# Optimization experiments

Hardware: AMD Instinct MI355X
Metric: run time of the kernel (lower is better)

The kernel has to match this reference:

```python
import jax, jax.numpy as jnp
import numpy as np

B = 4          # clouds per batch
N_PER = 8192   # points per cloud
RATIO = 0.5
M = int(N_PER * RATIO)   # sampled centroids per cloud
R = 0.2        # radius
K = 64         # max_num_neighbors
C_IN = 64


def setup_inputs() -> dict:
    key = jax.random.key(0)
    k1, k2, k3, k4 = jax.random.split(key, 4)
    N = B * N_PER
    x = jax.random.normal(k1, (N, C_IN), dtype=jnp.float32)
    pos = jax.random.uniform(k2, (N, 3), dtype=jnp.float32)  # unit cube
    batch = jnp.repeat(jnp.arange(B, dtype=jnp.int32), N_PER)
    W1 = jax.random.normal(k3, (C_IN + 3, 64), dtype=jnp.float32) * (1.0 / np.sqrt(C_IN + 3))
    b1 = jnp.zeros((64,), dtype=jnp.float32)
    W2 = jax.random.normal(k4, (64, 128), dtype=jnp.float32) * (1.0 / np.sqrt(64))
    b2 = jnp.zeros((128,), dtype=jnp.float32)
    return {"x": x, "pos": pos, "batch": batch, "W1": W1, "b1": b1, "W2": W2, "b2": b2}


def _fps(posb):
    """Farthest point sampling, vectorized over clouds. posb: [B, n, 3] -> idx [B, M]."""
    d0 = jnp.sum((posb - posb[:, :1]) ** 2, axis=-1)  # dist^2 to seed point 0: [B, n]

    def step(dists, _):
        far = jnp.argmax(dists, axis=1)                              # [B]
        newp = jnp.take_along_axis(posb, far[:, None, None], axis=1)  # [B, 1, 3]
        d = jnp.sum((posb - newp) ** 2, axis=-1)                      # [B, n]
        return jnp.minimum(dists, d), far.astype(jnp.int32)

    _, rest = jax.lax.scan(step, d0, None, length=M - 1)  # rest: [M-1, B]
    return jnp.concatenate([jnp.zeros((B, 1), jnp.int32), rest.T], axis=1)  # [B, M]


def reference(x, pos, batch, W1, b1, W2, b2):
    posb = pos.reshape(B, N_PER, 3)
    xb = x.reshape(B, N_PER, C_IN)

    # --- fps ---
    idx = _fps(posb)                                         # [B, M]
    q = jnp.take_along_axis(posb, idx[:, :, None], axis=1)   # sampled centroids [B, M, 3]

    # --- radius query: K nearest neighbors within radius R (same cloud) ---
    d2 = jnp.sum((q[:, :, None, :] - posb[:, None, :, :]) ** 2, axis=-1)  # [B, M, n]
    neg = jnp.where(d2 <= R * R, -d2, -jnp.inf)
    vals, nbr = jax.lax.top_k(neg, K)                        # [B, M, K]
    valid = vals > -jnp.inf                                  # neighbor mask

    # --- PointNetConv: gather -> MLP -> masked max aggregation ---
    bidx = jnp.arange(B)[:, None, None]
    xj = xb[bidx, nbr]                                       # [B, M, K, C_IN]
    rel = posb[bidx, nbr] - q[:, :, None, :]                 # [B, M, K, 3]
    feat = jnp.concatenate([xj, rel], axis=-1)               # [B, M, K, C_IN+3]
    h = jax.nn.relu(feat @ W1 + b1)                          # [B, M, K, 64]
    h = jax.nn.relu(h @ W2 + b2)                             # [B, M, K, 128]
    h = jnp.where(valid[..., None], h, -jnp.inf)
    out = jnp.max(h, axis=2)                                 # [B, M, 128]; self-edge guarantees >=1 valid

    x_out = out.reshape(B * M, 128)
    pos_out = q.reshape(B * M, 3)
    batch_out = jnp.repeat(jnp.arange(B, dtype=batch.dtype), M)
    return x_out, pos_out, batch_out
```

## Files before the change

### kernel.cpp

```cpp
#include <hip/hip_runtime.h>
#include <stdint.h>

#define NPER 8192
#define NB 4
#define MPER 4096
#define MTOT (NB*MPER)
#define KNB 64
#define CIN 64
#define R2C 0.04f

#define POSOUT_OFF (MTOT*128)
#define BATCH_OFF  (MTOT*128 + MTOT*3)

#define SSTR 30720

typedef float v2f __attribute__((ext_vector_type(2)));

#define FPS_T 1024
#define PTS 8
#define NCELL 512

#define OFF_XS 0
#define OFF_YS (OFF_XS + NPER*4)
#define OFF_ZS (OFF_YS + NPER*4)
#define OFF_OS (OFF_ZS + NPER*4)
#define OFF_WIN (OFF_OS + NPER*2)
#define OFF_HIST (OFF_WIN + MPER*2)
#define OFF_SCAN (OFF_HIST + NCELL*4)
#define OFF_SLOT (OFF_SCAN + NCELL*4)
#define OFF_SID0 (OFF_SLOT + 24)
#define FPS_LDS  (OFF_SID0 + 8)

template<int CTRL>
__device__ __forceinline__ unsigned dppmax(unsigned v) {
  unsigned t = (unsigned)__builtin_amdgcn_update_dpp(
      0, (int)v, CTRL, 0xf, 0xf, true);
  return v > t ? v : t;
}
__device__ __forceinline__ unsigned wave_max_u32(unsigned v) {
  v = dppmax<0x111>(v);
  v = dppmax<0x112>(v);
  v = dppmax<0x114>(v);
  v = dppmax<0x118>(v);
  v = dppmax<0x142>(v);
  v = dppmax<0x143>(v);
  return (unsigned)__builtin_amdgcn_readlane((int)v, 63);
}

__global__ __launch_bounds__(1024) void k_fps(const float* __restrict__ pos,
                                              float* __restrict__ dout)
{
#pragma clang fp contract(off)
  extern __shared__ char smem[];
  float* Xs = (float*)(smem + OFF_XS);
  float* Ys = (float*)(smem + OFF_YS);
  float* Zs = (float*)(smem + OFF_ZS);
  unsigned short* Os = (unsigned short*)(smem + OFF_OS);
  unsigned short* winb = (unsigned short*)(smem + OFF_WIN);
  unsigned* hist = (unsigned*)(smem + OFF_HIST);
  unsigned* scanb = (unsigned*)(smem + OFF_SCAN);
  unsigned long long* slot3 = (unsigned long long*)(smem + OFF_SLOT);
  unsigned* sid0p = (unsigned*)(smem + OFF_SID0);

  const int b = blockIdx.x;
  const int tid = threadIdx.x;
  const float* pb = pos + (size_t)b * NPER * 3;
  float* qo = dout + POSOUT_OFF + (size_t)b * MPER * 3;
  float* scrb = dout + (size_t)b * SSTR;
  float* gSX = scrb; float* gSY = scrb + 8192; float* gSZ = scrb + 16384;
  unsigned* gSO = (unsigned*)(scrb + 24576);
  unsigned* gCS = (unsigned*)(scrb + 28672);

  if (tid < NCELL) hist[tid] = 0u;
  if (tid == 0) { slot3[0] = 0ull; slot3[1] = 0ull; slot3[2] = 0ull; }
  __syncthreads();

  float sxv[PTS], syv[PTS], szv[PTS];
  unsigned cellv[PTS];
#pragma unroll
  for (int k = 0; k < PTS; ++k) {
    int i = k * FPS_T + tid;
    sxv[k] = pb[i*3+0]; syv[k] = pb[i*3+1]; szv[k] = pb[i*3+2];
    unsigned ix = min(7u, (unsigned)(int)(sxv[k] * 8.0f));
    unsigned iy = min(7u, (unsigned)(int)(syv[k] * 8.0f));
    unsigned iz = min(7u, (unsigned)(int)(szv[k] * 8.0f));
    cellv[k] = (ix << 6) | (iy << 3) | iz;
    atomicAdd(&hist[cellv[k]], 1u);
  }
  __syncthreads();
  if (tid < NCELL) scanb[tid] = hist[tid];
  __syncthreads();
  for (int s = 1; s < NCELL; s <<= 1) {
    unsigned v = 0u;
    if (tid >= s && tid < NCELL) v = scanb[tid - s];
    __syncthreads();
    if (tid >= s && tid < NCELL) scanb[tid] += v;
    __syncthreads();
  }
  if (tid < NCELL) {
    hist[tid] = scanb[tid] - hist[tid];
    gCS[tid+1] = scanb[tid];
  }
  if (tid == 0) gCS[0] = 0u;
  __syncthreads();
#pragma unroll
  for (int k = 0; k < PTS; ++k) {
    unsigned dst = atomicAdd(&hist[cellv[k]], 1u);
    int orig = k * FPS_T + tid;
    Xs[dst] = sxv[k]; Ys[dst] = syv[k]; Zs[dst] = szv[k];
    Os[dst] = (unsigned short)orig;
    if (orig == 0) *sid0p = dst;
  }
  __syncthreads();
  for (int e = tid; e < NPER; e += FPS_T) {
    gSX[e] = Xs[e]; gSY[e] = Ys[e]; gSZ[e] = Zs[e];
  }
  for (int e = tid; e < NPER/2; e += FPS_T)
    gSO[e] = ((const unsigned*)Os)[e];
  v2f Xp[4], Yp[4], Zp[4], Dp[4];
  unsigned RK[PTS];
  float bxlo = 3.402823466e+38f, bylo = bxlo, bzlo = bxlo;
  float bxhi = -bxlo, byhi = bxhi, bzhi = bxhi;
#pragma unroll
  for (int k = 0; k < PTS; ++k) {
    int s = tid * PTS + k;
    float xx = Xs[s], yy = Ys[s], zz = Zs[s];
    Xp[k>>1][k&1] = xx; Yp[k>>1][k&1] = yy; Zp[k>>1][k&1] = zz;
    Dp[k>>1][k&1] = 3.402823466e+38f;
    unsigned orig = Os[s];
    RK[k] = ((unsigned)(NPER - 1 - orig) << 13) | (unsigned)s;
    bxlo = fminf(bxlo, xx); bxhi = fmaxf(bxhi, xx);
    bylo = fminf(bylo, yy); byhi = fmaxf(byhi, yy);
    bzlo = fminf(bzlo, zz); bzhi = fmaxf(bzhi, zz);
  }

  unsigned long long tkey = 0ull, wkey = 0ull;
  float lmax = 3.402823466e+38f;
  unsigned sidx = *sid0p;
  for (int m = 1; m < MPER; ++m) {
    const float cx = Xs[sidx], cy = Ys[sidx], cz = Zs[sidx];
    if (tid == 0) winb[m-1] = (unsigned short)sidx;
    if (tid == 1) slot3[(m+1) % 3] = 0ull;
    float ax = fmaxf(fmaxf(__fsub_rn(bxlo, cx), __fsub_rn(cx, bxhi)), 0.0f);
    float ay = fmaxf(fmaxf(__fsub_rn(bylo, cy), __fsub_rn(cy, byhi)), 0.0f);
    float az = fmaxf(fmaxf(__fsub_rn(bzlo, cz), __fsub_rn(cz, bzhi)), 0.0f);
    float lb = ax*ax + ay*ay + az*az;
    bool upd = (lb * 0.99988f) < lmax;
    if (__ballot(upd) != 0ull) {
      if (upd) {
        v2f cx2 = {cx, cx}, cy2 = {cy, cy}, cz2 = {cz, cz};
        v2f dnp[4];
        float bd = -1.0f;
#pragma unroll
        for (int p = 0; p < 4; ++p) {
          v2f dx = Xp[p] - cx2;
          v2f dy = Yp[p] - cy2;
          v2f dz = Zp[p] - cz2;
          v2f s = (dx*dx + dy*dy) + dz*dz;
          v2f dn;
          dn.x = fminf(Dp[p].x, s.x);
          dn.y = fminf(Dp[p].y, s.y);
          Dp[p] = dn; dnp[p] = dn;
          bd = fmaxf(bd, fmaxf(dn.x, dn.y));
        }
        unsigned brk = 0u;
#pragma unroll
        for (int p = 0; p < 4; ++p) {
          brk = (dnp[p].x == bd) ? max(brk, RK[2*p])   : brk;
          brk = (dnp[p].y == bd) ? max(brk, RK[2*p+1]) : brk;
        }
        tkey = ((unsigned long long)__float_as_uint(bd) << 26) | brk;
        lmax = bd;
      }
      unsigned hi = (unsigned)(tkey >> 26);
      unsigned M = wave_max_u32(hi);
      unsigned rk = (unsigned)tkey & 0x3FFFFFFu;
      unsigned long long msk = __ballot(hi == M);
      unsigned lo;
      if (__popcll(msk) == 1) {
        int ln = (int)__builtin_ctzll(msk);
        lo = (unsigned)__builtin_amdgcn_readlane((int)rk, ln);
      } else {
        lo = wave_max_u32((hi == M) ? rk : 0u);
      }
      wkey = ((unsigned long long)M << 26) | lo;
    }
    if ((tid & 63) == 0) atomicMax(&slot3[m % 3], wkey);
    __syncthreads();
    sidx = (unsigned)(slot3[m % 3] & 0x1FFFull);
  }
  if (tid == 0) winb[MPER-1] = (unsigned short)sidx;
  __syncthreads();
  for (int e = tid; e < MPER; e += FPS_T) {
    unsigned s = winb[e];
    qo[e*3+0] = Xs[s]; qo[e*3+1] = Ys[s]; qo[e*3+2] = Zs[s];
  }
}

#define SCAP 512
__global__ __launch_bounds__(256) void k_radius(const float* __restrict__ pos,
    float* __restrict__ dout, unsigned short* __restrict__ nbr,
    int* __restrict__ cnt)
{
  __shared__ unsigned candH[4][SCAP];
  __shared__ unsigned candL[4][SCAP];
  const int wid = threadIdx.x >> 6, lane = threadIdx.x & 63;
  const int m = blockIdx.x * 4 + wid;
  const int b = m >> 12;
  const float* scrb = dout + (size_t)b * SSTR;
  const float* SX = scrb;
  const float* SY = scrb + 8192;
  const float* SZ = scrb + 16384;
  const unsigned short* SO = (const unsigned short*)(scrb + 24576);
  const unsigned* CS = (const unsigned*)(scrb + 28672);
  const float* q = dout + POSOUT_OFF + (size_t)m * 3;
  const float qx = q[0], qy = q[1], qz = q[2];
  const int ixc = min(7, (int)(qx * 8.0f));
  const int iyc = min(7, (int)(qy * 8.0f));
  const int izc = min(7, (int)(qz * 8.0f));
  const int izlo = max(izc-2, 0), izhi = min(izc+2, 7);
  unsigned s0v = 0u, s1v = 0u;
  {
    int ix = ixc + lane / 5 - 2;
    int iy = iyc + lane % 5 - 2;
    if (lane < 25 && ix >= 0 && ix < 8 && iy >= 0 && iy < 8) {
      int cb = (ix << 6) | (iy << 3);
      s0v = CS[cb + izlo];
      s1v = CS[cb + izhi + 1];
    }
  }
  unsigned cw = 0;
  for (int seg = 0; seg < 25; ++seg) {
    unsigned s0 = (unsigned)__builtin_amdgcn_readlane((int)s0v, seg);
    unsigned s1 = (unsigned)__builtin_amdgcn_readlane((int)s1v, seg);
    for (unsigned i0 = s0; i0 < s1; i0 += 64) {
      unsigned i = i0 + (unsigned)lane;
      float dx = __fsub_rn(qx, SX[i]);
      float dy = __fsub_rn(qy, SY[i]);
      float dz = __fsub_rn(qz, SZ[i]);
      float d2 = __fadd_rn(__fadd_rn(__fmul_rn(dx,dx), __fmul_rn(dy,dy)),
                           __fmul_rn(dz,dz));
      bool in = (i < s1) && (d2 <= R2C);
      unsigned long long mk = __ballot(in);
      unsigned pre = (unsigned)__popcll(mk & ((1ull << lane) - 1ull));
      if (in) {
        unsigned slot = cw + pre;
        if (slot < SCAP) {
          candH[wid][slot] = __float_as_uint(d2);
          candL[wid][slot] = (unsigned)SO[i];
        }
      }
      cw += (unsigned)__popcll(mk);
    }
  }
  if (cw > SCAP) cw = SCAP;
  for (int s = (int)cw + lane; s < SCAP; s += 64) {
    candH[wid][s] = 0xFFFFFFFFu; candL[wid][s] = 0xFFFFFFFFu;
  }
  __syncthreads();
  for (int k = 2; k <= SCAP; k <<= 1) {
    for (int j = k >> 1; j > 0; j >>= 1) {
#pragma unroll
      for (int s = 0; s < SCAP/128; ++s) {
        int t = lane + (s << 6);
        int e = ((t & ~(j-1)) << 1) | (t & (j-1));
        int p = e | j;
        unsigned aH = candH[wid][e], aL = candL[wid][e];
        unsigned cH = candH[wid][p], cL = candL[wid][p];
        bool agt = (aH > cH) || (aH == cH && aL > cL);
        bool asc = ((e & k) == 0);
        bool sw = asc ? agt : !agt && (aH != cH || aL != cL);
        if (sw) {
          candH[wid][e] = cH; candL[wid][e] = cL;
          candH[wid][p] = aH; candL[wid][p] = aL;
        }
      }
      __syncthreads();
    }
  }
  int kk = (int)cw; if (kk > KNB) kk = KNB;
  nbr[(size_t)m*KNB + lane] =
    (lane < kk) ? (unsigned short)(candL[wid][lane] & 0xFFFFu)
                : (unsigned short)0;
  if (lane == 0) {
    cnt[m] = kk;
    dout[BATCH_OFF + m] = (float)b;
  }
}

__global__ __launch_bounds__(128) void k_conv(
    const float* __restrict__ x, const float* __restrict__ pos,
    const float* __restrict__ W1, const float* __restrict__ b1,
    const float* __restrict__ W2, const float* __restrict__ b2,
    const unsigned short* __restrict__ nbr, const int* __restrict__ cntp,
    float* __restrict__ dout)
{
  __shared__ __align__(16) float bufA[68*68];
  __shared__ __align__(16) float bufB[68*68];
  __shared__ unsigned short nbr_s[64];
  __shared__ float qv[3];
  __shared__ int cnt_s;
  const int t = threadIdx.x;
  const int m = blockIdx.x;
  const int b = m >> 12;
  if (t < 64) nbr_s[t] = nbr[(size_t)m*KNB + t];
  else if (t == 64) cnt_s = cntp[m];
  else if (t >= 65 && t < 68) qv[t-65] = dout[POSOUT_OFF + (size_t)m*3 + (t-65)];
  for (int e = t; e < 67*64; e += 128) {
    int ch = e >> 6, h = e & 63;
    bufB[ch*68 + h] = W1[e];
  }
  __syncthreads();
  {
    const int ch = t & 63, jj = t >> 6;
    const size_t xb = (size_t)b * NPER * CIN;
    for (int j0 = 0; j0 < 64; j0 += 2) {
      int j = j0 + jj;
      int r = nbr_s[j];
      bufA[ch*68 + j] = x[xb + (size_t)r*CIN + ch];
    }
  }
  {
    const size_t pbb = (size_t)b * NPER * 3;
    for (int e = t; e < 192; e += 128) {
      int j = e & 63, d = e >> 6;
      int r = nbr_s[j];
      bufA[(64+d)*68 + j] = pos[pbb + (size_t)r*3 + d] - qv[d];
    }
  }
  __syncthreads();

  const int jg = t & 7, hg = t >> 3;
  const int j0 = jg << 3;
  const int h0 = hg << 2;
  float acc[4][8];
#pragma unroll
  for (int hh = 0; hh < 4; ++hh)
#pragma unroll
    for (int j = 0; j < 8; ++j) acc[hh][j] = 0.0f;
  for (int ch = 0; ch < 67; ++ch) {
    const float4 fa = *(const float4*)&bufA[ch*68 + j0];
    const float4 fb = *(const float4*)&bufA[ch*68 + j0 + 4];
    const float4 w  = *(const float4*)&bufB[ch*68 + h0];
    const float ws4[4] = {w.x, w.y, w.z, w.w};
    const float fj[8] = {fa.x, fa.y, fa.z, fa.w, fb.x, fb.y, fb.z, fb.w};
#pragma unroll
    for (int hh = 0; hh < 4; ++hh)
#pragma unroll
      for (int j = 0; j < 8; ++j)
        acc[hh][j] += ws4[hh] * fj[j];
  }
  __syncthreads();
  {
    const float4 bb = *(const float4*)&b1[h0];
    const float bv[4] = {bb.x, bb.y, bb.z, bb.w};
#pragma unroll
    for (int hh = 0; hh < 4; ++hh) {
      float4 o0, o1;
      o0.x = fmaxf(acc[hh][0] + bv[hh], 0.0f);
      o0.y = fmaxf(acc[hh][1] + bv[hh], 0.0f);
      o0.z = fmaxf(acc[hh][2] + bv[hh], 0.0f);
      o0.w = fmaxf(acc[hh][3] + bv[hh], 0.0f);
      o1.x = fmaxf(acc[hh][4] + bv[hh], 0.0f);
      o1.y = fmaxf(acc[hh][5] + bv[hh], 0.0f);
      o1.z = fmaxf(acc[hh][6] + bv[hh], 0.0f);
      o1.w = fmaxf(acc[hh][7] + bv[hh], 0.0f);
      *(float4*)&bufA[(h0+hh)*68 + j0] = o0;
      *(float4*)&bufA[(h0+hh)*68 + j0 + 4] = o1;
    }
  }
  const int c0 = hg << 3;
  float acc2[8][8];
#pragma unroll
  for (int c = 0; c < 8; ++c)
#pragma unroll
    for (int j = 0; j < 8; ++j) acc2[c][j] = 0.0f;
  for (int hc = 0; hc < 64; hc += 16) {
    __syncthreads();
    for (int e = t; e < 16*128; e += 128) {
      int hh = e >> 7, c = e & 127;
      bufB[hh*136 + c] = W2[(size_t)(hc+hh)*128 + c];
    }
    __syncthreads();
#pragma unroll
    for (int h = 0; h < 16; ++h) {
      const float4 ja = *(const float4*)&bufA[(hc+h)*68 + j0];
      const float4 jb = *(const float4*)&bufA[(hc+h)*68 + j0 + 4];
      const float4 wa = *(const float4*)&bufB[h*136 + c0];
      const float4 wb = *(const float4*)&bufB[h*136 + c0 + 4];
      const float hv[8] = {ja.x, ja.y, ja.z, ja.w, jb.x, jb.y, jb.z, jb.w};
      const float wv[8] = {wa.x, wa.y, wa.z, wa.w, wb.x, wb.y, wb.z, wb.w};
#pragma unroll
      for (int c = 0; c < 8; ++c)
#pragma unroll
        for (int j = 0; j < 8; ++j)
          acc2[c][j] += wv[c] * hv[j];
    }
  }
  const int cntv = cnt_s;
  const float4 b2a = *(const float4*)&b2[c0];
  const float4 b2b = *(const float4*)&b2[c0 + 4];
  const float bv2[8] = {b2a.x, b2a.y, b2a.z, b2a.w, b2b.x, b2b.y, b2b.z, b2b.w};
  float best[8];
#pragma unroll
  for (int c = 0; c < 8; ++c) {
    float v = -3.402823466e+38f;
#pragma unroll
    for (int j = 0; j < 8; ++j) {
      float hv = fmaxf(acc2[c][j] + bv2[c], 0.0f);
      v = (j0 + j < cntv) ? fmaxf(v, hv) : v;
    }
    best[c] = v;
  }
#pragma unroll
  for (int off = 1; off < 8; off <<= 1)
#pragma unroll
    for (int c = 0; c < 8; ++c)
      best[c] = fmaxf(best[c], __shfl_xor(best[c], off));
  if (jg == 0) {
    float4 o0 = {best[0], best[1], best[2], best[3]};
    float4 o1 = {best[4], best[5], best[6], best[7]};
    *(float4*)&dout[(size_t)m*128 + c0] = o0;
    *(float4*)&dout[(size_t)m*128 + c0 + 4] = o1;
  }
}

extern "C" void kernel_launch(void* const* d_in, const int* in_sizes, int n_in,
                              void* d_out, int out_size, void* d_ws, size_t ws_size,
                              hipStream_t stream) {
  const float* x   = (const float*)d_in[0];
  const float* pos = (const float*)d_in[1];
  const float* W1  = (const float*)d_in[3];
  const float* b1  = (const float*)d_in[4];
  const float* W2  = (const float*)d_in[5];
  const float* b2  = (const float*)d_in[6];
  float* dout = (float*)d_out;
  unsigned short* nbr = (unsigned short*)d_ws;
  int* cnt = (int*)((char*)d_ws + (size_t)MTOT*KNB*2);

  hipLaunchKernelGGL(k_fps,    dim3(NB),     dim3(FPS_T), FPS_LDS, stream, pos, dout);
  hipLaunchKernelGGL(k_radius, dim3(MTOT/4), dim3(256),   0, stream, pos, dout, nbr, cnt);
  hipLaunchKernelGGL(k_conv,   dim3(MTOT),   dim3(128),   0, stream,
                     x, pos, W1, b1, W2, b2, nbr, cnt, dout);
}
```

Baseline: 3.354 ms.

## Use bounding-sphere skip test in FPS, interleave xyz, pack MLP FMAs

The FPS loop replaces the per-thread AABB lower-bound test with a bounding-sphere test. It precomputes a threshold from the thread's max min-distance, so the skip check costs one squared distance against the sphere centre. Point coordinates in LDS move from three SoA arrays to an interleaved xyz array, so each centroid fetch reads adjacent words. The MLP kernel's two GEMM inner loops are rewritten with v2f accumulators to encourage packed FP32 FMA instructions. The sphere bound is looser than the box bound, so more threads may do the update step.

New measurement: 4.646 ms. 1.39x slower.

```diff
diff --git a/kernel.cpp b/kernel.cpp
--- a/kernel.cpp
+++ b/kernel.cpp
@@ -20,10 +20,8 @@
 #define PTS 8
 #define NCELL 512
 
-#define OFF_XS 0
-#define OFF_YS (OFF_XS + NPER*4)
-#define OFF_ZS (OFF_YS + NPER*4)
-#define OFF_OS (OFF_ZS + NPER*4)
+#define OFF_XYZ 0
+#define OFF_OS (OFF_XYZ + NPER*12)
 #define OFF_WIN (OFF_OS + NPER*2)
 #define OFF_HIST (OFF_WIN + MPER*2)
 #define OFF_SCAN (OFF_HIST + NCELL*4)
@@ -52,9 +50,7 @@
 {
 #pragma clang fp contract(off)
   extern __shared__ char smem[];
-  float* Xs = (float*)(smem + OFF_XS);
-  float* Ys = (float*)(smem + OFF_YS);
-  float* Zs = (float*)(smem + OFF_ZS);
+  float* xyz = (float*)(smem + OFF_XYZ);
   unsigned short* Os = (unsigned short*)(smem + OFF_OS);
   unsigned short* winb = (unsigned short*)(smem + OFF_WIN);
   unsigned* hist = (unsigned*)(smem + OFF_HIST);
@@ -107,13 +103,13 @@
   for (int k = 0; k < PTS; ++k) {
     unsigned dst = atomicAdd(&hist[cellv[k]], 1u);
     int orig = k * FPS_T + tid;
-    Xs[dst] = sxv[k]; Ys[dst] = syv[k]; Zs[dst] = szv[k];
+    xyz[dst*3+0] = sxv[k]; xyz[dst*3+1] = syv[k]; xyz[dst*3+2] = szv[k];
     Os[dst] = (unsigned short)orig;
     if (orig == 0) *sid0p = dst;
   }
   __syncthreads();
   for (int e = tid; e < NPER; e += FPS_T) {
-    gSX[e] = Xs[e]; gSY[e] = Ys[e]; gSZ[e] = Zs[e];
+    gSX[e] = xyz[e*3+0]; gSY[e] = xyz[e*3+1]; gSZ[e] = xyz[e*3+2];
   }
   for (int e = tid; e < NPER/2; e += FPS_T)
     gSO[e] = ((const unsigned*)Os)[e];
@@ -124,7 +120,7 @@
 #pragma unroll
   for (int k = 0; k < PTS; ++k) {
     int s = tid * PTS + k;
-    float xx = Xs[s], yy = Ys[s], zz = Zs[s];
+    float xx = xyz[s*3+0], yy = xyz[s*3+1], zz = xyz[s*3+2];
     Xp[k>>1][k&1] = xx; Yp[k>>1][k&1] = yy; Zp[k>>1][k&1] = zz;
     Dp[k>>1][k&1] = 3.402823466e+38f;
     unsigned orig = Os[s];
@@ -133,19 +129,23 @@
     bylo = fminf(bylo, yy); byhi = fmaxf(byhi, yy);
     bzlo = fminf(bzlo, zz); bzhi = fmaxf(bzhi, zz);
   }
+  const float scx = 0.5f*(bxlo+bxhi), scy = 0.5f*(bylo+byhi),
+              scz = 0.5f*(bzlo+bzhi);
+  float hx = __fsub_rn(bxhi, scx), hy = __fsub_rn(byhi, scy),
+        hz = __fsub_rn(bzhi, scz);
+  const float rr = sqrtf(hx*hx + hy*hy + hz*hz) * 1.0001f;
 
   unsigned long long tkey = 0ull, wkey = 0ull;
-  float lmax = 3.402823466e+38f;
+  float thr2 = 3.402823466e+38f;
   unsigned sidx = *sid0p;
   for (int m = 1; m < MPER; ++m) {
-    const float cx = Xs[sidx], cy = Ys[sidx], cz = Zs[sidx];
+    const unsigned ci = sidx * 3u;
+    const float cx = xyz[ci], cy = xyz[ci+1], cz = xyz[ci+2];
     if (tid == 0) winb[m-1] = (unsigned short)sidx;
     if (tid == 1) slot3[(m+1) % 3] = 0ull;
-    float ax = fmaxf(fmaxf(__fsub_rn(bxlo, cx), __fsub_rn(cx, bxhi)), 0.0f);
-    float ay = fmaxf(fmaxf(__fsub_rn(bylo, cy), __fsub_rn(cy, byhi)), 0.0f);
-    float az = fmaxf(fmaxf(__fsub_rn(bzlo, cz), __fsub_rn(cz, bzhi)), 0.0f);
-    float lb = ax*ax + ay*ay + az*az;
-    bool upd = (lb * 0.99988f) < lmax;
+    float dcx = cx - scx, dcy = cy - scy, dcz = cz - scz;
+    float dc2 = (dcx*dcx + dcy*dcy) + dcz*dcz;
+    bool upd = dc2 < thr2;
     if (__ballot(upd) != 0ull) {
       if (upd) {
         v2f cx2 = {cx, cx}, cy2 = {cy, cy}, cz2 = {cz, cz};
@@ -170,7 +170,8 @@
           brk = (dnp[p].y == bd) ? max(brk, RK[2*p+1]) : brk;
         }
         tkey = ((unsigned long long)__float_as_uint(bd) << 26) | brk;
-        lmax = bd;
+        float thr = rr + sqrtf(bd) * 1.0001f;
+        thr2 = thr * thr * 1.0001f;
       }
       unsigned hi = (unsigned)(tkey >> 26);
       unsigned M = wave_max_u32(hi);
@@ -193,7 +194,7 @@
   __syncthreads();
   for (int e = tid; e < MPER; e += FPS_T) {
     unsigned s = winb[e];
-    qo[e*3+0] = Xs[s]; qo[e*3+1] = Ys[s]; qo[e*3+2] = Zs[s];
+    qo[e*3+0] = xyz[s*3+0]; qo[e*3+1] = xyz[s*3+1]; qo[e*3+2] = xyz[s*3+2];
   }
 }
 
@@ -333,22 +334,24 @@
   const int jg = t & 7, hg = t >> 3;
   const int j0 = jg << 3;
   const int h0 = hg << 2;
-  float acc[4][8];
+  v2f accp[4][4];
 #pragma unroll
   for (int hh = 0; hh < 4; ++hh)
 #pragma unroll
-    for (int j = 0; j < 8; ++j) acc[hh][j] = 0.0f;
+    for (int jp = 0; jp < 4; ++jp) accp[hh][jp] = (v2f){0.0f, 0.0f};
   for (int ch = 0; ch < 67; ++ch) {
     const float4 fa = *(const float4*)&bufA[ch*68 + j0];
     const float4 fb = *(const float4*)&bufA[ch*68 + j0 + 4];
     const float4 w  = *(const float4*)&bufB[ch*68 + h0];
+    const v2f fj[4] = {{fa.x, fa.y}, {fa.z, fa.w}, {fb.x, fb.y}, {fb.z, fb.w}};
     const float ws4[4] = {w.x, w.y, w.z, w.w};
-    const float fj[8] = {fa.x, fa.y, fa.z, fa.w, fb.x, fb.y, fb.z, fb.w};
-#pragma unroll
-    for (int hh = 0; hh < 4; ++hh)
-#pragma unroll
-      for (int j = 0; j < 8; ++j)
-        acc[hh][j] += ws4[hh] * fj[j];
+#pragma unroll
+    for (int hh = 0; hh < 4; ++hh) {
+      const v2f wv2 = {ws4[hh], ws4[hh]};
+#pragma unroll
+      for (int jp = 0; jp < 4; ++jp)
+        accp[hh][jp] += wv2 * fj[jp];
+    }
   }
   __syncthreads();
   {
@@ -357,24 +360,24 @@
 #pragma unroll
     for (int hh = 0; hh < 4; ++hh) {
       float4 o0, o1;
-      o0.x = fmaxf(acc[hh][0] + bv[hh], 0.0f);
-      o0.y = fmaxf(acc[hh][1] + bv[hh], 0.0f);
-      o0.z = fmaxf(acc[hh][2] + bv[hh], 0.0f);
-      o0.w = fmaxf(acc[hh][3] + bv[hh], 0.0f);
-      o1.x = fmaxf(acc[hh][4] + bv[hh], 0.0f);
-      o1.y = fmaxf(acc[hh][5] + bv[hh], 0.0f);
-      o1.z = fmaxf(acc[hh][6] + bv[hh], 0.0f);
-      o1.w = fmaxf(acc[hh][7] + bv[hh], 0.0f);
+      o0.x = fmaxf(accp[hh][0].x + bv[hh], 0.0f);
+      o0.y = fmaxf(accp[hh][0].y + bv[hh], 0.0f);
+      o0.z = fmaxf(accp[hh][1].x + bv[hh], 0.0f);
+      o0.w = fmaxf(accp[hh][1].y + bv[hh], 0.0f);
+      o1.x = fmaxf(accp[hh][2].x + bv[hh], 0.0f);
+      o1.y = fmaxf(accp[hh][2].y + bv[hh], 0.0f);
+      o1.z = fmaxf(accp[hh][3].x + bv[hh], 0.0f);
+      o1.w = fmaxf(accp[hh][3].y + bv[hh], 0.0f);
       *(float4*)&bufA[(h0+hh)*68 + j0] = o0;
       *(float4*)&bufA[(h0+hh)*68 + j0 + 4] = o1;
     }
   }
   const int c0 = hg << 3;
-  float acc2[8][8];
+  v2f acc2p[8][4];
 #pragma unroll
   for (int c = 0; c < 8; ++c)
 #pragma unroll
-    for (int j = 0; j < 8; ++j) acc2[c][j] = 0.0f;
+    for (int jp = 0; jp < 4; ++jp) acc2p[c][jp] = (v2f){0.0f, 0.0f};
   for (int hc = 0; hc < 64; hc += 16) {
     __syncthreads();
     for (int e = t; e < 16*128; e += 128) {
@@ -388,13 +391,15 @@
       const float4 jb = *(const float4*)&bufA[(hc+h)*68 + j0 + 4];
       const float4 wa = *(const float4*)&bufB[h*136 + c0];
       const float4 wb = *(const float4*)&bufB[h*136 + c0 + 4];
-      const float hv[8] = {ja.x, ja.y, ja.z, ja.w, jb.x, jb.y, jb.z, jb.w};
+      const v2f hj[4] = {{ja.x, ja.y}, {ja.z, ja.w}, {jb.x, jb.y}, {jb.z, jb.w}};
       const float wv[8] = {wa.x, wa.y, wa.z, wa.w, wb.x, wb.y, wb.z, wb.w};
 #pragma unroll
-      for (int c = 0; c < 8; ++c)
-#pragma unroll
-        for (int j = 0; j < 8; ++j)
-          acc2[c][j] += wv[c] * hv[j];
+      for (int c = 0; c < 8; ++c) {
+        const v2f w2 = {wv[c], wv[c]};
+#pragma unroll
+        for (int jp = 0; jp < 4; ++jp)
+          acc2p[c][jp] += w2 * hj[jp];
+      }
     }
   }
   const int cntv = cnt_s;
@@ -406,9 +411,11 @@
   for (int c = 0; c < 8; ++c) {
     float v = -3.402823466e+38f;
 #pragma unroll
-    for (int j = 0; j < 8; ++j) {
-      float hv = fmaxf(acc2[c][j] + bv2[c], 0.0f);
-      v = (j0 + j < cntv) ? fmaxf(v, hv) : v;
+    for (int jp = 0; jp < 4; ++jp) {
+      float h0v = fmaxf(acc2p[c][jp].x + bv2[c], 0.0f);
+      float h1v = fmaxf(acc2p[c][jp].y + bv2[c], 0.0f);
+      v = (j0 + 2*jp     < cntv) ? fmaxf(v, h0v) : v;
+      v = (j0 + 2*jp + 1 < cntv) ? fmaxf(v, h1v) : v;
     }
     best[c] = v;
   }
```
